# Kernel optimization log

Hardware: AMD Instinct MI355X
Metric: run time of the kernel (lower is better)

## Reference

```python
import jax, jax.numpy as jnp
import numpy as np

D_DIM, H_DIM, W_DIM = 8, 16, 16
HIDDEN, HEAD = 256, 32
NUM_HEADS = HIDDEN // HEAD


def _rel_indices(D, H, W):
    # 3D relative coordinate indices into the bias table, shape (N, N) each.
    coords = np.stack(np.meshgrid(np.arange(D), np.arange(H), np.arange(W), indexing='ij'),
                      axis=-1).reshape(-1, 3)
    rel = coords[:, None, :] - coords[None, :, :]
    rel[:, :, 0] += D - 1
    rel[:, :, 1] += H - 1
    rel[:, :, 2] += W - 1
    return jnp.asarray(rel[:, :, 0]), jnp.asarray(rel[:, :, 1]), jnp.asarray(rel[:, :, 2])


def setup_inputs() -> dict:
    key = jax.random.key(0)
    ks = jax.random.split(key, 6)
    B = 4
    x = jax.random.normal(ks[0], (B, D_DIM, H_DIM, W_DIM, HIDDEN), dtype=jnp.float32)
    s = 1.0 / np.sqrt(HIDDEN)
    Wq = jax.random.normal(ks[1], (HIDDEN, HIDDEN), dtype=jnp.float32) * s
    Wk = jax.random.normal(ks[2], (HIDDEN, HIDDEN), dtype=jnp.float32) * s
    Wv = jax.random.normal(ks[3], (HIDDEN, HIDDEN), dtype=jnp.float32) * s
    Wo = jax.random.normal(ks[4], (HIDDEN, HIDDEN), dtype=jnp.float32) * s
    bias_table = jax.random.normal(ks[5], (NUM_HEADS, 2 * D_DIM - 1, 2 * H_DIM - 1, 2 * W_DIM - 1),
                                   dtype=jnp.float32) * 0.02
    return {"x": x, "Wq": Wq, "Wk": Wk, "Wv": Wv, "Wo": Wo, "bias_table": bias_table}


def reference(x, Wq, Wk, Wv, Wo, bias_table):
    B, D, H, W, C = x.shape
    N = D * H * W
    rd, rh, rw = _rel_indices(D, H, W)
    # gathered relative-position bias: (num_heads, N, N)
    bias = bias_table[:, rd, rh, rw]

    xf = x.reshape(B, N, C)
    q = (xf @ Wq).reshape(B, N, NUM_HEADS, HEAD).transpose(0, 2, 1, 3)  # b h n d
    k = (xf @ Wk).reshape(B, N, NUM_HEADS, HEAD).transpose(0, 2, 1, 3)
    v = (xf @ Wv).reshape(B, N, NUM_HEADS, HEAD).transpose(0, 2, 1, 3)

    scores = jnp.einsum('bhnd,bhmd->bhnm', q, k) / jnp.sqrt(jnp.float32(HEAD))
    scores = scores + bias[None]  # broadcast over batch
    attn = jax.nn.softmax(scores, axis=-1)
    out = jnp.einsum('bhnm,bhmd->bhnd', attn, v)
    out = out.transpose(0, 2, 1, 3).reshape(B, N, HIDDEN) @ Wo
    return out.reshape(B, D, H, W, HIDDEN)
```

## Files before the change

kernel.cpp:

```cpp
#include <hip/hip_runtime.h>
#include <math.h>

#define HIDDEN 256
#define NHEADS 8
#define HEAD 32
#define NTOK 2048
#define NBIAS 115320
#define HTAB 14415

typedef __attribute__((ext_vector_type(8))) __bf16 bf16x8;
typedef __attribute__((ext_vector_type(4))) float f32x4;
typedef __attribute__((ext_vector_type(16))) float f32x16;
typedef __attribute__((ext_vector_type(4))) unsigned uint32x4;

static __device__ __forceinline__ f32x4 mfma16(bf16x8 a, bf16x8 b, f32x4 c) {
    return __builtin_amdgcn_mfma_f32_16x16x32_bf16(a, b, c, 0, 0, 0);
}
static __device__ __forceinline__ f32x16 mfma32(bf16x8 a, bf16x8 b, f32x16 c) {
    return __builtin_amdgcn_mfma_f32_32x32x16_bf16(a, b, c, 0, 0, 0);
}
static __device__ __forceinline__ float fexp2(float x) {
#if __has_builtin(__builtin_amdgcn_exp2f)
    return __builtin_amdgcn_exp2f(x);
#else
    return exp2f(x);
#endif
}
static __device__ __forceinline__ unsigned pkbf16(float a, float b) {
    unsigned short ua = __builtin_bit_cast(unsigned short, (__bf16)a);
    unsigned short ub = __builtin_bit_cast(unsigned short, (__bf16)b);
    return (unsigned)ua | ((unsigned)ub << 16);
}

__global__ void k_cvt_x(const float* __restrict__ x, __bf16* __restrict__ xb) {
    int i = (blockIdx.x * blockDim.x + threadIdx.x) * 4;
    float4 v = *(const float4*)(x + i);
    xb[i + 0] = (__bf16)v.x;
    xb[i + 1] = (__bf16)v.y;
    xb[i + 2] = (__bf16)v.z;
    xb[i + 3] = (__bf16)v.w;
}

__global__ void k_cvt_w(const float* __restrict__ w0, const float* __restrict__ w1,
                        const float* __restrict__ w2, const float* __restrict__ w3,
                        __bf16* __restrict__ t0, __bf16* __restrict__ t1,
                        __bf16* __restrict__ t2, __bf16* __restrict__ t3) {
    int wsel = blockIdx.x >> 8;
    int i = (blockIdx.x & 255) * 256 + threadIdx.x;
    const float* w = (wsel == 0) ? w0 : (wsel == 1) ? w1 : (wsel == 2) ? w2 : w3;
    __bf16* t = (wsel == 0) ? t0 : (wsel == 1) ? t1 : (wsel == 2) ? t2 : t3;
    int n = i >> 8, k = i & 255;
    t[i] = (__bf16)w[k * 256 + n];
}

__global__ __launch_bounds__(256) void k_qkv(const __bf16* __restrict__ xb,
                                             const __bf16* __restrict__ wqT,
                                             const __bf16* __restrict__ wkT,
                                             const __bf16* __restrict__ wvT,
                                             __bf16* __restrict__ qb,
                                             __bf16* __restrict__ kb,
                                             __bf16* __restrict__ vb) {
    int wid = blockIdx.x * 4 + (threadIdx.x >> 6);
    int lane = threadIdx.x & 63;
    int ng = wid % 12, mt = wid / 12;
    int lm = lane & 15, lg = lane >> 4, lk = lg * 8;
    int which = ng >> 2;
    int nc0 = (ng & 3) * 64;
    const __bf16* wT = (which == 0) ? wqT : (which == 1) ? wkT : wvT;

    f32x4 acc[4][4];
#pragma unroll
    for (int m = 0; m < 4; ++m)
#pragma unroll
        for (int n = 0; n < 4; ++n) acc[m][n] = (f32x4){0.f, 0.f, 0.f, 0.f};

    const __bf16* arow = xb + (size_t)(mt * 64 + lm) * 256 + lk;
    const __bf16* brow = wT + (size_t)(nc0 + lm) * 256 + lk;
#pragma unroll
    for (int kk = 0; kk < 8; ++kk) {
        bf16x8 a[4], b[4];
#pragma unroll
        for (int m = 0; m < 4; ++m) a[m] = *(const bf16x8*)(arow + (size_t)m * 16 * 256 + kk * 32);
#pragma unroll
        for (int n = 0; n < 4; ++n) b[n] = *(const bf16x8*)(brow + (size_t)n * 16 * 256 + kk * 32);
#pragma unroll
        for (int m = 0; m < 4; ++m)
#pragma unroll
            for (int n = 0; n < 4; ++n) acc[m][n] = mfma16(a[m], b[n], acc[m][n]);
    }
    const float QS = 0.17677669529663687f * 1.4426950408889634f;
#pragma unroll
    for (int m = 0; m < 4; ++m) {
#pragma unroll
        for (int n = 0; n < 4; ++n) {
            int col = nc0 + n * 16 + lm;
            int h = col >> 5, d = col & 31;
#pragma unroll
            for (int r = 0; r < 4; ++r) {
                int row = mt * 64 + m * 16 + lg * 4 + r;
                int b_ = row >> 11, tr = row & 2047;
                size_t bh = (size_t)(b_ * 8 + h) * 65536;
                if (which == 0) {
                    qb[bh + (size_t)tr * 32 + d] = (__bf16)(acc[m][n][r] * QS);
                } else if (which == 1) {
                    size_t idx = ((size_t)(tr >> 5) * 128 + (d >> 4) * 64 + ((d >> 3) & 1) * 32 + (tr & 31)) * 8 + (d & 7);
                    kb[bh + idx] = (__bf16)acc[m][n][r];
                } else {
                    size_t idx = ((size_t)(tr >> 5) * 256 + ((tr >> 3) & 3) * 64 + ((tr >> 2) & 1) * 32 + d) * 4 + (tr & 3);
                    vb[bh + idx] = (__bf16)acc[m][n][r];
                }
            }
        }
    }
}

__global__ __launch_bounds__(256) void k_attn(const __bf16* __restrict__ qb,
                                              const __bf16* __restrict__ kb,
                                              const __bf16* __restrict__ vb,
                                              const float* __restrict__ bias,
                                              __bf16* __restrict__ attn) {
    int i = blockIdx.x;
    int x = i & 7, r_ = i >> 3;
    int bh = x + ((r_ >> 5) << 3);
    int qblk = r_ & 31;
    int b_ = bh >> 3, h = bh & 7;
    int w = threadIdx.x >> 6;
    int lane = threadIdx.x & 63;
    int lq = lane & 31;
    int hf = lane >> 5;
    int q0 = qblk * 64;

    __shared__ float smem[5016];

    {
        int qd = q0 >> 8, qh0 = (q0 >> 4) & 15;
        const float* bt = bias + h * HTAB;
        for (int t = threadIdx.x; t < 5016; t += 256) {
            int dd = t / 627, rem = t - dd * 627;
            int hh = rem / 33, ww = rem - hh * 33;
            int dw = 30 - ww; if (dw < 0) dw = 0;
            smem[t] = bt[(qd + dd) * 961 + (qh0 + hh) * 31 + dw] * 1.4426950408889634f;
        }
    }
    __syncthreads();

    const __bf16* qbase = qb + (size_t)bh * NTOK * 32;
    const __bf16* kbase = kb + (size_t)bh * NTOK * 32;
    const __bf16* vbase = vb + (size_t)bh * NTOK * 32;

    bf16x8 qfA0 = *(const bf16x8*)(qbase + (size_t)(q0 + lq) * 32 + hf * 8);
    bf16x8 qfA1 = *(const bf16x8*)(qbase + (size_t)(q0 + lq) * 32 + 16 + hf * 8);
    bf16x8 qfB0 = *(const bf16x8*)(qbase + (size_t)(q0 + 32 + lq) * 32 + hf * 8);
    bf16x8 qfB1 = *(const bf16x8*)(qbase + (size_t)(q0 + 32 + lq) * 32 + 16 + hf * 8);

    int lbase = (lq >> 4) * 33 + 15 - (lq & 15) + 4 * hf;

    f32x16 OaccA, LaccA, OaccB, LaccB;
#pragma unroll
    for (int j = 0; j < 16; ++j) { OaccA[j] = 0.f; LaccA[j] = 0.f; OaccB[j] = 0.f; LaccB[j] = 0.f; }

    bf16x8 ones;
#pragma unroll
    for (int j = 0; j < 8; ++j) ones[j] = (__bf16)1.0f;

    bf16x8 ck0, ck1;
    {
        const __bf16* kt = kbase + ((size_t)(w * 16) * 128 + lane) * 8;
        ck0 = *(const bf16x8*)(kt);
        ck1 = *(const bf16x8*)(kt + 512);
    }

#pragma unroll
    for (int it = 0; it < 16; ++it) {
        int t0 = w * 512 + it * 32;
        int tt = t0 >> 5;

        bf16x8 nk0, nk1;
        if (it < 15) {
            const __bf16* kt1 = kbase + ((size_t)(tt + 1) * 128 + lane) * 8;
            nk0 = *(const bf16x8*)(kt1);
            nk1 = *(const bf16x8*)(kt1 + 512);
        }

        const __bf16* vt = vbase + ((size_t)tt * 256 + lane) * 4;
        uint2 va  = *(const uint2*)(vt);
        uint2 vbq = *(const uint2*)(vt + 256);
        uint2 vc  = *(const uint2*)(vt + 512);
        uint2 vd  = *(const uint2*)(vt + 768);
        uint32x4 vw0 = {va.x, va.y, vbq.x, vbq.y};
        uint32x4 vw1 = {vc.x, vc.y, vd.x, vd.y};
        bf16x8 vf0 = __builtin_bit_cast(bf16x8, vw0);
        bf16x8 vf1 = __builtin_bit_cast(bf16x8, vw1);

        int kd = t0 >> 8, kh0 = (t0 >> 4) & 15;
        int a0 = (7 - kd) * 627 + (15 - kh0) * 33 + lbase;
        f32x16 SA, SB;
#pragma unroll
        for (int r = 0; r < 4; ++r) {
            SA[r]      = smem[a0 + r];
            SA[4 + r]  = smem[a0 + 8 + r];
            SA[8 + r]  = smem[a0 - 33 + r];
            SA[12 + r] = smem[a0 - 25 + r];
            SB[r]      = smem[a0 + 66 + r];
            SB[4 + r]  = smem[a0 + 74 + r];
            SB[8 + r]  = smem[a0 + 33 + r];
            SB[12 + r] = smem[a0 + 41 + r];
        }
        SA = mfma32(ck0, qfA0, SA);
        SA = mfma32(ck1, qfA1, SA);
        SB = mfma32(ck0, qfB0, SB);
        SB = mfma32(ck1, qfB1, SB);

        {
            unsigned W0 = pkbf16(fexp2(SA[0]),  fexp2(SA[1]));
            unsigned W1 = pkbf16(fexp2(SA[2]),  fexp2(SA[3]));
            unsigned W2 = pkbf16(fexp2(SA[4]),  fexp2(SA[5]));
            unsigned W3 = pkbf16(fexp2(SA[6]),  fexp2(SA[7]));
            unsigned W4 = pkbf16(fexp2(SA[8]),  fexp2(SA[9]));
            unsigned W5 = pkbf16(fexp2(SA[10]), fexp2(SA[11]));
            unsigned W6 = pkbf16(fexp2(SA[12]), fexp2(SA[13]));
            unsigned W7 = pkbf16(fexp2(SA[14]), fexp2(SA[15]));
            uint32x4 pw0 = {W0, W1, W2, W3};
            uint32x4 pw1 = {W4, W5, W6, W7};
            bf16x8 pf0 = __builtin_bit_cast(bf16x8, pw0);
            bf16x8 pf1 = __builtin_bit_cast(bf16x8, pw1);
            OaccA = mfma32(vf0, pf0, OaccA);
            OaccA = mfma32(vf1, pf1, OaccA);
            LaccA = mfma32(ones, pf0, LaccA);
            LaccA = mfma32(ones, pf1, LaccA);
        }
        {
            unsigned W0 = pkbf16(fexp2(SB[0]),  fexp2(SB[1]));
            unsigned W1 = pkbf16(fexp2(SB[2]),  fexp2(SB[3]));
            unsigned W2 = pkbf16(fexp2(SB[4]),  fexp2(SB[5]));
            unsigned W3 = pkbf16(fexp2(SB[6]),  fexp2(SB[7]));
            unsigned W4 = pkbf16(fexp2(SB[8]),  fexp2(SB[9]));
            unsigned W5 = pkbf16(fexp2(SB[10]), fexp2(SB[11]));
            unsigned W6 = pkbf16(fexp2(SB[12]), fexp2(SB[13]));
            unsigned W7 = pkbf16(fexp2(SB[14]), fexp2(SB[15]));
            uint32x4 pw0 = {W0, W1, W2, W3};
            uint32x4 pw1 = {W4, W5, W6, W7};
            bf16x8 pf0 = __builtin_bit_cast(bf16x8, pw0);
            bf16x8 pf1 = __builtin_bit_cast(bf16x8, pw1);
            OaccB = mfma32(vf0, pf0, OaccB);
            OaccB = mfma32(vf1, pf1, OaccB);
            LaccB = mfma32(ones, pf0, LaccB);
            LaccB = mfma32(ones, pf1, LaccB);
        }

        if (it < 15) { ck0 = nk0; ck1 = nk1; }
    }

    float (*part)[64][17] = (float (*)[64][17])smem;
#pragma unroll
    for (int s = 0; s < 2; ++s) {
        f32x16* O = s ? &OaccB : &OaccA;
        f32x16* L = s ? &LaccB : &LaccA;
        __syncthreads();
#pragma unroll
        for (int j = 0; j < 4; ++j) {
            float4 t;
            t.x = (*O)[4 * j]; t.y = (*O)[4 * j + 1]; t.z = (*O)[4 * j + 2]; t.w = (*O)[4 * j + 3];
            *(float4*)&part[w][lane][4 * j] = t;
        }
        part[w][lane][16] = (*L)[0];
        __syncthreads();

        float4 o = {0.f, 0.f, 0.f, 0.f};
        float ls = 0.f;
#pragma unroll
        for (int sw = 0; sw < 4; ++sw) {
            float4 t = *(const float4*)&part[sw][lane][4 * w];
            o.x += t.x; o.y += t.y; o.z += t.z; o.w += t.w;
            ls += part[sw][lane][16];
        }
        float inv = 1.0f / ls;
        unsigned lo = pkbf16(o.x * inv, o.y * inv);
        unsigned hi = pkbf16(o.z * inv, o.w * inv);
        size_t base = ((size_t)b_ * NTOK + q0 + 32 * s + lq) * 256 + h * 32 + 8 * w + 4 * hf;
        *(uint2*)(attn + base) = make_uint2(lo, hi);
    }
}

__global__ __launch_bounds__(256) void k_out(const __bf16* __restrict__ attn,
                                             const __bf16* __restrict__ woT,
                                             float* __restrict__ out) {
    int wid = blockIdx.x * 4 + (threadIdx.x >> 6);
    int lane = threadIdx.x & 63;
    int ng = wid & 3, mt = wid >> 2;
    int lm = lane & 15, lg = lane >> 4, lk = lg * 8;
    int nc0 = ng * 64;

    f32x4 acc[4][4];
#pragma unroll
    for (int m = 0; m < 4; ++m)
#pragma unroll
        for (int n = 0; n < 4; ++n) acc[m][n] = (f32x4){0.f, 0.f, 0.f, 0.f};

    const __bf16* arow = attn + (size_t)(mt * 64 + lm) * 256 + lk;
    const __bf16* brow = woT + (size_t)(nc0 + lm) * 256 + lk;
#pragma unroll
    for (int kk = 0; kk < 8; ++kk) {
        bf16x8 a[4], b[4];
#pragma unroll
        for (int m = 0; m < 4; ++m) a[m] = *(const bf16x8*)(arow + (size_t)m * 16 * 256 + kk * 32);
#pragma unroll
        for (int n = 0; n < 4; ++n) b[n] = *(const bf16x8*)(brow + (size_t)n * 16 * 256 + kk * 32);
#pragma unroll
        for (int m = 0; m < 4; ++m)
#pragma unroll
            for (int n = 0; n < 4; ++n) acc[m][n] = mfma16(a[m], b[n], acc[m][n]);
    }
#pragma unroll
    for (int m = 0; m < 4; ++m) {
#pragma unroll
        for (int n = 0; n < 4; ++n) {
            int col = nc0 + n * 16 + lm;
#pragma unroll
            for (int r = 0; r < 4; ++r) {
                int row = mt * 64 + m * 16 + lg * 4 + r;
                out[(size_t)row * 256 + col] = acc[m][n][r];
            }
        }
    }
}

extern "C" void kernel_launch(void* const* d_in, const int* in_sizes, int n_in,
                              void* d_out, int out_size, void* d_ws, size_t ws_size,
                              hipStream_t stream) {
    const float* x    = (const float*)d_in[0];
    const float* Wq   = (const float*)d_in[1];
    const float* Wk   = (const float*)d_in[2];
    const float* Wv   = (const float*)d_in[3];
    const float* Wo   = (const float*)d_in[4];
    const float* bias = (const float*)d_in[5];
    float* out = (float*)d_out;

    __bf16* ws  = (__bf16*)d_ws;
    __bf16* xb  = ws;
    __bf16* wqT = xb  + 2097152;
    __bf16* wkT = wqT + 65536;
    __bf16* wvT = wkT + 65536;
    __bf16* woT = wvT + 65536;
    __bf16* qb  = woT + 65536;
    __bf16* kb  = qb  + 2097152;
    __bf16* vb  = kb  + 2097152;
    __bf16* att = xb;

    k_cvt_x<<<2048, 256, 0, stream>>>(x, xb);
    k_cvt_w<<<1024, 256, 0, stream>>>(Wq, Wk, Wv, Wo, wqT, wkT, wvT, woT);
    k_qkv<<<384, 256, 0, stream>>>(xb, wqT, wkT, wvT, qb, kb, vb);
    k_attn<<<1024, 256, 0, stream>>>(qb, kb, vb, bias, att);
    k_out<<<128, 256, 0, stream>>>(att, woT, out);
}
```

Baseline: 84.17 us.

## Fuse conversion kernels, stage K/V stores via LDS, prefetch bias, split out GEMM

Merges the x and weight conversion kernels into a single launch to save one kernel launch. The QKV projection becomes one wave per block, and K/V results are staged through shared memory so the swizzled global stores become 16-byte vector writes instead of scattered scalar writes. The attention loop loads the next tile's relative-position bias from LDS one iteration ahead to hide LDS latency. The output GEMM halves the rows per wave and doubles the grid for more parallelism, in exchange for reloading weight tiles more often.

Result: faster. 78.17 us (-7.1%).

```diff
diff --git a/kernel.cpp b/kernel.cpp
--- a/kernel.cpp
+++ b/kernel.cpp
@@ -32,36 +32,39 @@
     return (unsigned)ua | ((unsigned)ub << 16);
 }
 
-__global__ void k_cvt_x(const float* __restrict__ x, __bf16* __restrict__ xb) {
-    int i = (blockIdx.x * blockDim.x + threadIdx.x) * 4;
-    float4 v = *(const float4*)(x + i);
-    xb[i + 0] = (__bf16)v.x;
-    xb[i + 1] = (__bf16)v.y;
-    xb[i + 2] = (__bf16)v.z;
-    xb[i + 3] = (__bf16)v.w;
-}
-
-__global__ void k_cvt_w(const float* __restrict__ w0, const float* __restrict__ w1,
-                        const float* __restrict__ w2, const float* __restrict__ w3,
-                        __bf16* __restrict__ t0, __bf16* __restrict__ t1,
-                        __bf16* __restrict__ t2, __bf16* __restrict__ t3) {
-    int wsel = blockIdx.x >> 8;
-    int i = (blockIdx.x & 255) * 256 + threadIdx.x;
-    const float* w = (wsel == 0) ? w0 : (wsel == 1) ? w1 : (wsel == 2) ? w2 : w3;
-    __bf16* t = (wsel == 0) ? t0 : (wsel == 1) ? t1 : (wsel == 2) ? t2 : t3;
-    int n = i >> 8, k = i & 255;
-    t[i] = (__bf16)w[k * 256 + n];
-}
-
-__global__ __launch_bounds__(256) void k_qkv(const __bf16* __restrict__ xb,
-                                             const __bf16* __restrict__ wqT,
-                                             const __bf16* __restrict__ wkT,
-                                             const __bf16* __restrict__ wvT,
-                                             __bf16* __restrict__ qb,
-                                             __bf16* __restrict__ kb,
-                                             __bf16* __restrict__ vb) {
-    int wid = blockIdx.x * 4 + (threadIdx.x >> 6);
-    int lane = threadIdx.x & 63;
+__global__ void k_prep(const float* __restrict__ x, const float* __restrict__ w0,
+                       const float* __restrict__ w1, const float* __restrict__ w2,
+                       const float* __restrict__ w3, __bf16* __restrict__ xb,
+                       __bf16* __restrict__ t0, __bf16* __restrict__ t1,
+                       __bf16* __restrict__ t2, __bf16* __restrict__ t3) {
+    int bid = blockIdx.x;
+    if (bid < 2048) {
+        int i = (bid * 256 + threadIdx.x) * 4;
+        float4 v = *(const float4*)(x + i);
+        xb[i + 0] = (__bf16)v.x;
+        xb[i + 1] = (__bf16)v.y;
+        xb[i + 2] = (__bf16)v.z;
+        xb[i + 3] = (__bf16)v.w;
+    } else {
+        int q = bid - 2048;
+        int wsel = q >> 8;
+        int i = (q & 255) * 256 + threadIdx.x;
+        const float* w = (wsel == 0) ? w0 : (wsel == 1) ? w1 : (wsel == 2) ? w2 : w3;
+        __bf16* t = (wsel == 0) ? t0 : (wsel == 1) ? t1 : (wsel == 2) ? t2 : t3;
+        int n = i >> 8, k = i & 255;
+        t[i] = (__bf16)w[k * 256 + n];
+    }
+}
+
+__global__ __launch_bounds__(64) void k_qkv(const __bf16* __restrict__ xb,
+                                            const __bf16* __restrict__ wqT,
+                                            const __bf16* __restrict__ wkT,
+                                            const __bf16* __restrict__ wvT,
+                                            __bf16* __restrict__ qb,
+                                            __bf16* __restrict__ kb,
+                                            __bf16* __restrict__ vb) {
+    int wid = blockIdx.x;
+    int lane = threadIdx.x;
     int ng = wid % 12, mt = wid / 12;
     int lm = lane & 15, lg = lane >> 4, lk = lg * 8;
     int which = ng >> 2;
@@ -88,29 +91,75 @@
 #pragma unroll
             for (int n = 0; n < 4; ++n) acc[m][n] = mfma16(a[m], b[n], acc[m][n]);
     }
-    const float QS = 0.17677669529663687f * 1.4426950408889634f;
-#pragma unroll
-    for (int m = 0; m < 4; ++m) {
-#pragma unroll
-        for (int n = 0; n < 4; ++n) {
-            int col = nc0 + n * 16 + lm;
-            int h = col >> 5, d = col & 31;
+
+    int b_ = mt >> 5;
+    int tb = (mt & 31) * 2;
+    int h0 = nc0 >> 5;
+
+    __shared__ __attribute__((aligned(16))) __bf16 tile[4608];
+
+    if (which == 0) {
+        const float QS = 0.17677669529663687f * 1.4426950408889634f;
+#pragma unroll
+        for (int m = 0; m < 4; ++m)
+#pragma unroll
+            for (int n = 0; n < 4; ++n) {
+                int col = nc0 + n * 16 + lm;
+                int h = col >> 5, d = col & 31;
+#pragma unroll
+                for (int r = 0; r < 4; ++r) {
+                    int row = mt * 64 + m * 16 + lg * 4 + r;
+                    qb[(size_t)(b_ * 8 + h) * 65536 + (size_t)(row & 2047) * 32 + d] =
+                        (__bf16)(acc[m][n][r] * QS);
+                }
+            }
+        return;
+    }
+
+#pragma unroll
+    for (int m = 0; m < 4; ++m)
+#pragma unroll
+        for (int n = 0; n < 4; ++n)
 #pragma unroll
             for (int r = 0; r < 4; ++r) {
-                int row = mt * 64 + m * 16 + lg * 4 + r;
-                int b_ = row >> 11, tr = row & 2047;
-                size_t bh = (size_t)(b_ * 8 + h) * 65536;
-                if (which == 0) {
-                    qb[bh + (size_t)tr * 32 + d] = (__bf16)(acc[m][n][r] * QS);
-                } else if (which == 1) {
-                    size_t idx = ((size_t)(tr >> 5) * 128 + (d >> 4) * 64 + ((d >> 3) & 1) * 32 + (tr & 31)) * 8 + (d & 7);
-                    kb[bh + idx] = (__bf16)acc[m][n][r];
-                } else {
-                    size_t idx = ((size_t)(tr >> 5) * 256 + ((tr >> 3) & 3) * 64 + ((tr >> 2) & 1) * 32 + d) * 4 + (tr & 3);
-                    vb[bh + idx] = (__bf16)acc[m][n][r];
+                int row = m * 16 + lg * 4 + r;
+                int col = n * 16 + lm;
+                if (which == 1) tile[row * 72 + col] = (__bf16)acc[m][n][r];
+                else            tile[col * 72 + row] = (__bf16)acc[m][n][r];
+            }
+    __syncthreads();
+
+    if (which == 1) {
+#pragma unroll
+        for (int tl = 0; tl < 2; ++tl)
+#pragma unroll
+            for (int hl = 0; hl < 2; ++hl) {
+                size_t gb = (size_t)(b_ * 8 + h0 + hl) * 65536 + (size_t)(tb + tl) * 1024;
+#pragma unroll
+                for (int half = 0; half < 2; ++half) {
+                    int u = half * 64 + lane;
+                    int j = u >> 6, hf2 = (u >> 5) & 1, lq2 = u & 31;
+                    bf16x8 vv = *(const bf16x8*)&tile[(tl * 32 + lq2) * 72 + hl * 32 + 16 * j + 8 * hf2];
+                    *(bf16x8*)(kb + gb + (size_t)u * 8) = vv;
                 }
             }
-        }
+    } else {
+#pragma unroll
+        for (int tl = 0; tl < 2; ++tl)
+#pragma unroll
+            for (int hl = 0; hl < 2; ++hl) {
+                size_t gb = (size_t)(b_ * 8 + h0 + hl) * 65536 + (size_t)(tb + tl) * 1024;
+#pragma unroll
+                for (int half = 0; half < 2; ++half) {
+                    int u0 = (half * 64 + lane) * 2;
+                    int g = u0 >> 6, hf2 = (u0 >> 5) & 1, d0 = u0 & 31;
+                    const __bf16* pl = &tile[(hl * 32 + d0) * 72 + tl * 32 + 8 * g + 4 * hf2];
+                    uint2 lo = *(const uint2*)pl;
+                    uint2 hi = *(const uint2*)(pl + 72);
+                    uint32x4 sv = {lo.x, lo.y, hi.x, hi.y};
+                    *(uint32x4*)(vb + gb + (size_t)u0 * 4) = sv;
+                }
+            }
     }
 }
 
@@ -163,6 +212,19 @@
 #pragma unroll
     for (int j = 0; j < 8; ++j) ones[j] = (__bf16)1.0f;
 
+    f32x16 bA, bB;
+    {
+        int t0 = w * 512;
+        int a0 = (7 - (t0 >> 8)) * 627 + (15 - ((t0 >> 4) & 15)) * 33 + lbase;
+#pragma unroll
+        for (int r = 0; r < 4; ++r) {
+            bA[r] = smem[a0 + r];      bA[4 + r] = smem[a0 + 8 + r];
+            bA[8 + r] = smem[a0 - 33 + r]; bA[12 + r] = smem[a0 - 25 + r];
+            bB[r] = smem[a0 + 66 + r]; bB[4 + r] = smem[a0 + 74 + r];
+            bB[8 + r] = smem[a0 + 33 + r]; bB[12 + r] = smem[a0 + 41 + r];
+        }
+    }
+
     bf16x8 ck0, ck1;
     {
         const __bf16* kt = kbase + ((size_t)(w * 16) * 128 + lane) * 8;
@@ -192,24 +254,23 @@
         bf16x8 vf0 = __builtin_bit_cast(bf16x8, vw0);
         bf16x8 vf1 = __builtin_bit_cast(bf16x8, vw1);
 
-        int kd = t0 >> 8, kh0 = (t0 >> 4) & 15;
-        int a0 = (7 - kd) * 627 + (15 - kh0) * 33 + lbase;
-        f32x16 SA, SB;
-#pragma unroll
-        for (int r = 0; r < 4; ++r) {
-            SA[r]      = smem[a0 + r];
-            SA[4 + r]  = smem[a0 + 8 + r];
-            SA[8 + r]  = smem[a0 - 33 + r];
-            SA[12 + r] = smem[a0 - 25 + r];
-            SB[r]      = smem[a0 + 66 + r];
-            SB[4 + r]  = smem[a0 + 74 + r];
-            SB[8 + r]  = smem[a0 + 33 + r];
-            SB[12 + r] = smem[a0 + 41 + r];
-        }
+        f32x16 SA = bA, SB = bB;
         SA = mfma32(ck0, qfA0, SA);
         SA = mfma32(ck1, qfA1, SA);
         SB = mfma32(ck0, qfB0, SB);
         SB = mfma32(ck1, qfB1, SB);
+
+        if (it < 15) {
+            int t1 = t0 + 32;
+            int a0 = (7 - (t1 >> 8)) * 627 + (15 - ((t1 >> 4) & 15)) * 33 + lbase;
+#pragma unroll
+            for (int r = 0; r < 4; ++r) {
+                bA[r] = smem[a0 + r];      bA[4 + r] = smem[a0 + 8 + r];
+                bA[8 + r] = smem[a0 - 33 + r]; bA[12 + r] = smem[a0 - 25 + r];
+                bB[r] = smem[a0 + 66 + r]; bB[4 + r] = smem[a0 + 74 + r];
+                bB[8 + r] = smem[a0 + 33 + r]; bB[12 + r] = smem[a0 + 41 + r];
+            }
+        }
 
         {
             unsigned W0 = pkbf16(fexp2(SA[0]),  fexp2(SA[1]));
@@ -291,34 +352,34 @@
     int lm = lane & 15, lg = lane >> 4, lk = lg * 8;
     int nc0 = ng * 64;
 
-    f32x4 acc[4][4];
-#pragma unroll
-    for (int m = 0; m < 4; ++m)
+    f32x4 acc[2][4];
+#pragma unroll
+    for (int m = 0; m < 2; ++m)
 #pragma unroll
         for (int n = 0; n < 4; ++n) acc[m][n] = (f32x4){0.f, 0.f, 0.f, 0.f};
 
-    const __bf16* arow = attn + (size_t)(mt * 64 + lm) * 256 + lk;
+    const __bf16* arow = attn + (size_t)(mt * 32 + lm) * 256 + lk;
     const __bf16* brow = woT + (size_t)(nc0 + lm) * 256 + lk;
 #pragma unroll
     for (int kk = 0; kk < 8; ++kk) {
-        bf16x8 a[4], b[4];
-#pragma unroll
-        for (int m = 0; m < 4; ++m) a[m] = *(const bf16x8*)(arow + (size_t)m * 16 * 256 + kk * 32);
+        bf16x8 a[2], b[4];
+#pragma unroll
+        for (int m = 0; m < 2; ++m) a[m] = *(const bf16x8*)(arow + (size_t)m * 16 * 256 + kk * 32);
 #pragma unroll
         for (int n = 0; n < 4; ++n) b[n] = *(const bf16x8*)(brow + (size_t)n * 16 * 256 + kk * 32);
 #pragma unroll
-        for (int m = 0; m < 4; ++m)
+        for (int m = 0; m < 2; ++m)
 #pragma unroll
             for (int n = 0; n < 4; ++n) acc[m][n] = mfma16(a[m], b[n], acc[m][n]);
     }
 #pragma unroll
-    for (int m = 0; m < 4; ++m) {
+    for (int m = 0; m < 2; ++m) {
 #pragma unroll
         for (int n = 0; n < 4; ++n) {
             int col = nc0 + n * 16 + lm;
 #pragma unroll
             for (int r = 0; r < 4; ++r) {
-                int row = mt * 64 + m * 16 + lg * 4 + r;
+                int row = mt * 32 + m * 16 + lg * 4 + r;
                 out[(size_t)row * 256 + col] = acc[m][n][r];
             }
         }
@@ -347,9 +408,8 @@
     __bf16* vb  = kb  + 2097152;
     __bf16* att = xb;
 
-    k_cvt_x<<<2048, 256, 0, stream>>>(x, xb);
-    k_cvt_w<<<1024, 256, 0, stream>>>(Wq, Wk, Wv, Wo, wqT, wkT, wvT, woT);
-    k_qkv<<<384, 256, 0, stream>>>(xb, wqT, wkT, wvT, qb, kb, vb);
+    k_prep<<<3072, 256, 0, stream>>>(x, Wq, Wk, Wv, Wo, xb, wqT, wkT, wvT, woT);
+    k_qkv<<<1536, 64, 0, stream>>>(xb, wqT, wkT, wvT, qb, kb, vb);
     k_attn<<<1024, 256, 0, stream>>>(qb, kb, vb, bias, att);
-    k_out<<<128, 256, 0, stream>>>(att, woT, out);
-}
+    k_out<<<256, 256, 0, stream>>>(att, woT, out);
+}
```
